# Performance work log

Measured on AMD Instinct MI355X. Metric: run time of the kernel, lower is better.

Reference implementation:

```python
import jax, jax.numpy as jnp
import numpy as np

EPS = 1e-5

def layer_norm(x, w, b):
    m = jnp.mean(x, axis=-1, keepdims=True)
    v = jnp.mean(jnp.square(x - m), axis=-1, keepdims=True)
    return (x - m) * jax.lax.rsqrt(v + EPS) * w + b

def time_shift(x):
    # shift sequence right by one, zero-pad first step: (B,L,D)
    return jnp.pad(x[:, :-1], ((0, 0), (1, 0), (0, 0)))

def wkv(time_decay, time_first, k, v):
    # Numerically-stable RWKV v4 WKV recurrence. k,v: (B,L,D)
    w = -jnp.exp(time_decay)  # (D,) negative decay
    u = time_first            # (D,)
    B, L, D = k.shape
    kT = jnp.swapaxes(k, 0, 1)  # (L,B,D)
    vT = jnp.swapaxes(v, 0, 1)
    a0 = jnp.zeros((B, D), k.dtype)
    b0 = jnp.zeros((B, D), k.dtype)
    p0 = jnp.full((B, D), -1e38, k.dtype)

    def step(carry, kv_t):
        a, b, p = carry
        k_t, v_t = kv_t
        ww = u + k_t
        q = jnp.maximum(p, ww)
        e1 = jnp.exp(p - q)
        e2 = jnp.exp(ww - q)
        out = (e1 * a + e2 * v_t) / (e1 * b + e2)
        ww2 = p + w
        q2 = jnp.maximum(ww2, k_t)
        e1b = jnp.exp(ww2 - q2)
        e2b = jnp.exp(k_t - q2)
        return (e1b * a + e2b * v_t, e1b * b + e2b, q2), out

    _, outs = jax.lax.scan(step, (a0, b0, p0), (kT, vT))
    return jnp.swapaxes(outs, 0, 1)  # (B,L,D)

def setup_inputs() -> dict:
    key = jax.random.key(0)
    B, L, D, D_att, D_ffn = 8, 2048, 1024, 1024, 4096
    ks = jax.random.split(key, 16)
    s = 1.0 / np.sqrt(D)
    inp = {
        "x": jax.random.normal(ks[0], (B, L, D), jnp.float32),
        "ln_att_w": jnp.ones((D,), jnp.float32),
        "ln_att_b": jnp.zeros((D,), jnp.float32),
        "ln_ffn_w": jnp.ones((D,), jnp.float32),
        "ln_ffn_b": jnp.zeros((D,), jnp.float32),
        "att_time_decay": jax.random.normal(ks[1], (D_att,), jnp.float32) * 0.5,
        "att_time_first": jax.random.normal(ks[2], (D_att,), jnp.float32) * 0.5,
        "att_mix_k": jax.random.uniform(ks[3], (D,), jnp.float32),
        "att_mix_v": jax.random.uniform(ks[4], (D,), jnp.float32),
        "att_mix_r": jax.random.uniform(ks[5], (D,), jnp.float32),
        "att_Wk": jax.random.normal(ks[6], (D_att, D), jnp.float32) * s,
        "att_Wv": jax.random.normal(ks[7], (D_att, D), jnp.float32) * s,
        "att_Wr": jax.random.normal(ks[8], (D_att, D), jnp.float32) * s,
        "att_Wo": jax.random.normal(ks[9], (D, D_att), jnp.float32) * s,
        "ffn_mix_k": jax.random.uniform(ks[10], (D,), jnp.float32),
        "ffn_mix_r": jax.random.uniform(ks[11], (D,), jnp.float32),
        "ffn_Wk": jax.random.normal(ks[12], (D_ffn, D), jnp.float32) * s,
        "ffn_Wv": jax.random.normal(ks[13], (D, D_ffn), jnp.float32) * (1.0 / np.sqrt(D_ffn)),
        "ffn_Wr": jax.random.normal(ks[14], (D, D), jnp.float32) * s,
    }
    return inp

def rwkv_block(x, ln_att_w, ln_att_b, ln_ffn_w, ln_ffn_b,
               att_time_decay, att_time_first, att_mix_k, att_mix_v, att_mix_r,
               att_Wk, att_Wv, att_Wr, att_Wo,
               ffn_mix_k, ffn_mix_r, ffn_Wk, ffn_Wv, ffn_Wr):
    # --- time-mix (WKV attention) ---
    xa = layer_norm(x, ln_att_w, ln_att_b)
    xs = time_shift(xa)
    k = jnp.einsum('bld,ad->bla', xa * att_mix_k + xs * (1.0 - att_mix_k), att_Wk)
    v = jnp.einsum('bld,ad->bla', xa * att_mix_v + xs * (1.0 - att_mix_v), att_Wv)
    r = jnp.einsum('bld,ad->bla', xa * att_mix_r + xs * (1.0 - att_mix_r), att_Wr)
    att = jnp.einsum('bla,da->bld', jax.nn.sigmoid(r) * wkv(att_time_decay, att_time_first, k, v), att_Wo)
    x = x + att
    # --- channel-mix FFN ---
    xf = layer_norm(x, ln_ffn_w, ln_ffn_b)
    xs = time_shift(xf)
    kx = xf * ffn_mix_k + xs * (1.0 - ffn_mix_k)
    rx = xf * ffn_mix_r + xs * (1.0 - ffn_mix_r)
    h = jnp.square(jax.nn.relu(jnp.einsum('bld,fd->blf', kx, ffn_Wk)))
    ffn = jax.nn.sigmoid(jnp.einsum('bld,ed->ble', rx, ffn_Wr)) * jnp.einsum('blf,df->bld', h, ffn_Wv)
    return x + ffn

def reference(x, ln_att_w, ln_att_b, ln_ffn_w, ln_ffn_b,
              att_time_decay, att_time_first, att_mix_k, att_mix_v, att_mix_r,
              att_Wk, att_Wv, att_Wr, att_Wo,
              ffn_mix_k, ffn_mix_r, ffn_Wk, ffn_Wv, ffn_Wr):
    return rwkv_block(x, ln_att_w, ln_att_b, ln_ffn_w, ln_ffn_b,
                      att_time_decay, att_time_first, att_mix_k, att_mix_v, att_mix_r,
                      att_Wk, att_Wv, att_Wr, att_Wo,
                      ffn_mix_k, ffn_mix_r, ffn_Wk, ffn_Wv, ffn_Wr)
```

## Files before the change

kernel.cpp:

```cpp
#include <hip/hip_runtime.h>
#include <stdint.h>

#define DDIM 1024
#define LSEQ 2048
#define BSZ  8
#define FDIM 4096
#define MROWS (BSZ*LSEQ)
#define NCHUNK 32
#define CLEN  (LSEQ/NCHUNK)

typedef float        f32x4  __attribute__((ext_vector_type(4)));
typedef unsigned int u32x4  __attribute__((ext_vector_type(4)));

using gas_void = const __attribute__((address_space(1))) void;
using las_void = __attribute__((address_space(3))) void;

__device__ __forceinline__ void gload16(const void* g, void* l) {
    __builtin_amdgcn_global_load_lds((gas_void*)g, (las_void*)l, 16, 0, 0);
}

__device__ __forceinline__ void mfma_bf16(f32x4& d, u32x4 a, u32x4 b) {
    asm("v_mfma_f32_16x16x32_bf16 %0, %1, %2, %0" : "+v"(d) : "v"(a), "v"(b));
}

__device__ __forceinline__ unsigned short f2bf(float f) {
    __bf16 h = (__bf16)f;
    return __builtin_bit_cast(unsigned short, h);
}

struct CvtArgs {
    const float* s[7];
    __bf16*      d[7];
    int          cum[8];
};

__global__ __launch_bounds__(256) void cvt_all(CvtArgs a)
{
    const int i = blockIdx.x * 256 + threadIdx.x;
    if (i >= a.cum[7]) return;
    int seg = 0;
#pragma unroll 6
    while (i >= a.cum[seg + 1]) ++seg;
    const int off = i - a.cum[seg];
    float4 f = ((const float4*)a.s[seg])[off];
    ushort4 o;
    o.x = f2bf(f.x); o.y = f2bf(f.y); o.z = f2bf(f.z); o.w = f2bf(f.w);
    ((ushort4*)a.d[seg])[off] = o;
}

__device__ __forceinline__ void blk_reduce4(float& a, float& b, float& c, float& d) {
#pragma unroll
    for (int off = 32; off >= 1; off >>= 1) {
        a += __shfl_xor(a, off, 64);
        b += __shfl_xor(b, off, 64);
        c += __shfl_xor(c, off, 64);
        d += __shfl_xor(d, off, 64);
    }
    __shared__ float sm[4][4];
    const int tid = threadIdx.x;
    if ((tid & 63) == 0) {
        sm[tid >> 6][0] = a; sm[tid >> 6][1] = b;
        sm[tid >> 6][2] = c; sm[tid >> 6][3] = d;
    }
    __syncthreads();
    a = sm[0][0] + sm[1][0] + sm[2][0] + sm[3][0];
    b = sm[0][1] + sm[1][1] + sm[2][1] + sm[3][1];
    c = sm[0][2] + sm[1][2] + sm[2][2] + sm[3][2];
    d = sm[0][3] + sm[1][3] + sm[2][3] + sm[3][3];
}

__global__ __launch_bounds__(256) void ln_mix3(
    const float* __restrict__ xin, const float* __restrict__ lnw, const float* __restrict__ lnb,
    const float* __restrict__ mkv, const float* __restrict__ mvv, const float* __restrict__ mrv,
    __bf16* __restrict__ ok, __bf16* __restrict__ ov, __bf16* __restrict__ orr)
{
    const int row = blockIdx.x;
    const int l   = row & (LSEQ - 1);
    const int tid = threadIdx.x;
    const size_t rbase = (size_t)row * DDIM;
    const float4 cur = ((const float4*)(xin + rbase))[tid];
    float4 prv = make_float4(0.f, 0.f, 0.f, 0.f);
    if (l > 0) prv = ((const float4*)(xin + rbase - DDIM))[tid];
    float s0 = cur.x + cur.y + cur.z + cur.w;
    float q0 = cur.x*cur.x + cur.y*cur.y + cur.z*cur.z + cur.w*cur.w;
    float s1 = prv.x + prv.y + prv.z + prv.w;
    float q1 = prv.x*prv.x + prv.y*prv.y + prv.z*prv.z + prv.w*prv.w;
    blk_reduce4(s0, q0, s1, q1);
    const float inv = 1.f / (float)DDIM;
    const float m0 = s0 * inv, m1 = s1 * inv;
    const float r0 = rsqrtf(fmaxf(q0 * inv - m0*m0, 0.f) + 1e-5f);
    const float r1 = rsqrtf(fmaxf(q1 * inv - m1*m1, 0.f) + 1e-5f);
    const float4 w4 = ((const float4*)lnw)[tid];
    const float4 b4 = ((const float4*)lnb)[tid];
    const float4 k4 = ((const float4*)mkv)[tid];
    const float4 v4 = ((const float4*)mvv)[tid];
    const float4 r4 = ((const float4*)mrv)[tid];
    const float cA[4] = {cur.x, cur.y, cur.z, cur.w};
    const float pA[4] = {prv.x, prv.y, prv.z, prv.w};
    const float wA[4] = {w4.x, w4.y, w4.z, w4.w};
    const float bA[4] = {b4.x, b4.y, b4.z, b4.w};
    const float kA[4] = {k4.x, k4.y, k4.z, k4.w};
    const float vA[4] = {v4.x, v4.y, v4.z, v4.w};
    const float rA[4] = {r4.x, r4.y, r4.z, r4.w};
    ushort4 pk, pv, pr;
    unsigned short* pkp = &pk.x; unsigned short* pvp = &pv.x; unsigned short* prp = &pr.x;
#pragma unroll
    for (int j = 0; j < 4; ++j) {
        float xa = (cA[j] - m0) * r0 * wA[j] + bA[j];
        float xs = (l > 0) ? ((pA[j] - m1) * r1 * wA[j] + bA[j]) : 0.f;
        pkp[j] = f2bf(xa * kA[j] + xs * (1.f - kA[j]));
        pvp[j] = f2bf(xa * vA[j] + xs * (1.f - vA[j]));
        prp[j] = f2bf(xa * rA[j] + xs * (1.f - rA[j]));
    }
    const size_t oi = (size_t)row * (DDIM/4) + tid;
    ((ushort4*)ok)[oi]  = pk;
    ((ushort4*)ov)[oi]  = pv;
    ((ushort4*)orr)[oi] = pr;
}

__global__ __launch_bounds__(256) void ln_mix2(
    const float* __restrict__ xin, const float* __restrict__ lnw, const float* __restrict__ lnb,
    const float* __restrict__ mkv, const float* __restrict__ mrv,
    __bf16* __restrict__ ok, __bf16* __restrict__ orr)
{
    const int row = blockIdx.x;
    const int l   = row & (LSEQ - 1);
    const int tid = threadIdx.x;
    const size_t rbase = (size_t)row * DDIM;
    const float4 cur = ((const float4*)(xin + rbase))[tid];
    float4 prv = make_float4(0.f, 0.f, 0.f, 0.f);
    if (l > 0) prv = ((const float4*)(xin + rbase - DDIM))[tid];
    float s0 = cur.x + cur.y + cur.z + cur.w;
    float q0 = cur.x*cur.x + cur.y*cur.y + cur.z*cur.z + cur.w*cur.w;
    float s1 = prv.x + prv.y + prv.z + prv.w;
    float q1 = prv.x*prv.x + prv.y*prv.y + prv.z*prv.z + prv.w*prv.w;
    blk_reduce4(s0, q0, s1, q1);
    const float inv = 1.f / (float)DDIM;
    const float m0 = s0 * inv, m1 = s1 * inv;
    const float r0 = rsqrtf(fmaxf(q0 * inv - m0*m0, 0.f) + 1e-5f);
    const float r1 = rsqrtf(fmaxf(q1 * inv - m1*m1, 0.f) + 1e-5f);
    const float4 w4 = ((const float4*)lnw)[tid];
    const float4 b4 = ((const float4*)lnb)[tid];
    const float4 k4 = ((const float4*)mkv)[tid];
    const float4 r4 = ((const float4*)mrv)[tid];
    const float cA[4] = {cur.x, cur.y, cur.z, cur.w};
    const float pA[4] = {prv.x, prv.y, prv.z, prv.w};
    const float wA[4] = {w4.x, w4.y, w4.z, w4.w};
    const float bA[4] = {b4.x, b4.y, b4.z, b4.w};
    const float kA[4] = {k4.x, k4.y, k4.z, k4.w};
    const float rA[4] = {r4.x, r4.y, r4.z, r4.w};
    ushort4 pk, pr;
    unsigned short* pkp = &pk.x; unsigned short* prp = &pr.x;
#pragma unroll
    for (int j = 0; j < 4; ++j) {
        float xa = (cA[j] - m0) * r0 * wA[j] + bA[j];
        float xs = (l > 0) ? ((pA[j] - m1) * r1 * wA[j] + bA[j]) : 0.f;
        pkp[j] = f2bf(xa * kA[j] + xs * (1.f - kA[j]));
        prp[j] = f2bf(xa * rA[j] + xs * (1.f - rA[j]));
    }
    const size_t oi = (size_t)row * (DDIM/4) + tid;
    ((ushort4*)ok)[oi]  = pk;
    ((ushort4*)orr)[oi] = pr;
}

__global__ __launch_bounds__(256) void wkv_phase1(
    const __bf16* __restrict__ kin, const __bf16* __restrict__ vin,
    const float* __restrict__ td,
    float* __restrict__ sa, float* __restrict__ sb, float* __restrict__ sp)
{
    const int idx = blockIdx.x * 256 + threadIdx.x;
    const int d  = idx & (DDIM - 1);
    const int bc = idx >> 10;
    const int b  = bc & (BSZ - 1);
    const int c  = bc >> 3;
    const float w = -__expf(td[d]);
    const size_t base = ((size_t)b * LSEQ + (size_t)c * CLEN) * DDIM + d;
    float a = 0.f, bbv = 0.f, p = -1e38f;
    for (int t = 0; t < CLEN; ++t) {
        const size_t off = base + (size_t)t * DDIM;
        const float kt = (float)kin[off];
        const float vt = (float)vin[off];
        const float ww2 = p + w;
        const float q2  = fmaxf(ww2, kt);
        const float e1  = __expf(ww2 - q2);
        const float e2  = __expf(kt - q2);
        a   = e1 * a   + e2 * vt;
        bbv = e1 * bbv + e2;
        p   = q2;
    }
    sa[idx] = a; sb[idx] = bbv; sp[idx] = p;
}

__global__ __launch_bounds__(256) void wkv_phase2(
    const __bf16* __restrict__ kin, const __bf16* __restrict__ vin,
    const __bf16* __restrict__ srin,
    const float* __restrict__ td, const float* __restrict__ tf,
    const float* __restrict__ sa, const float* __restrict__ sb,
    const float* __restrict__ sp,
    __bf16* __restrict__ outp)
{
    const int idx = blockIdx.x * 256 + threadIdx.x;
    const int d  = idx & (DDIM - 1);
    const int bc = idx >> 10;
    const int b  = bc & (BSZ - 1);
    const int c  = bc >> 3;
    const float w = -__expf(td[d]);
    const float u = tf[d];
    const float nw = (float)CLEN * w;

    float a = 0.f, bbv = 0.f, p = -1e38f;
    for (int j = 0; j < c; ++j) {
        const int sidx = ((j * BSZ + b) << 10) + d;
        const float aj = sa[sidx], bj = sb[sidx], pj = sp[sidx];
        const float ps = p + nw;
        const float pn = fmaxf(ps, pj);
        const float e1 = __expf(ps - pn);
        const float e2 = __expf(pj - pn);
        a   = e1 * a   + e2 * aj;
        bbv = e1 * bbv + e2 * bj;
        p   = pn;
    }

    const size_t base = ((size_t)b * LSEQ + (size_t)c * CLEN) * DDIM + d;
    for (int t = 0; t < CLEN; ++t) {
        const size_t off = base + (size_t)t * DDIM;
        const float kt = (float)kin[off];
        const float vt = (float)vin[off];
        const float sr = (float)srin[off];
        const float ww = u + kt;
        const float q  = fmaxf(p, ww);
        const float e1 = __expf(p - q);
        const float e2 = __expf(ww - q);
        const float o  = (e1 * a + e2 * vt) / (e1 * bbv + e2);
        outp[off] = (__bf16)(sr * o);
        const float ww2 = p + w;
        const float q2  = fmaxf(ww2, kt);
        const float e1b = __expf(ww2 - q2);
        const float e2b = __expf(kt - q2);
        a   = e1b * a   + e2b * vt;
        bbv = e1b * bbv + e2b;
        p   = q2;
    }
}

template<int EPI>
__global__ __launch_bounds__(512, 2)
void gemm8(const __bf16* __restrict__ A, const __bf16* __restrict__ Bw,
           float* outF, __bf16* outH,
           const float* auxF, const __bf16* __restrict__ auxH,
           int N, int K, int gy)
{
    __shared__ __align__(16) char smem[131072];
    const int tid  = threadIdx.x;
    const int lane = tid & 63;
    const int wid  = tid >> 6;
    const int wr = wid >> 2, wc = wid & 3;

    const int nwg = gridDim.x;
    const int f = blockIdx.x;
    const int g = (f & 7) * (nwg >> 3) + (f >> 3);
    const int tx = g / gy;
    const int ty = g - tx * gy;
    const size_t row0 = (size_t)tx * 256;
    const size_t col0 = (size_t)ty * 256;

    auto stage = [&](int buf, int k0, int isB, int q) {
        const int row  = q * 128 + (tid >> 2);
        const int slot = (tid & 3) ^ ((row >> 1) & 3);
        const __bf16* gp = (isB ? Bw + (col0 + row) * (size_t)K
                                : A  + (row0 + row) * (size_t)K) + k0 + slot * 8;
        char* lp = smem + buf * 32768 + isB * 16384 + q * 8192 + wid * 1024;
        gload16(gp, lp);
    };
    auto rdA = [&](int buf, int m) -> u32x4 {
        const int row  = wr * 128 + m * 16 + (lane & 15);
        const int slot = (lane >> 4) ^ ((row >> 1) & 3);
        return *(const u32x4*)(smem + buf * 32768 + row * 64 + slot * 16);
    };
    auto rdB = [&](int buf, int n) -> u32x4 {
        const int row  = wc * 64 + n * 16 + (lane & 15);
        const int slot = (lane >> 4) ^ ((row >> 1) & 3);
        return *(const u32x4*)(smem + buf * 32768 + 16384 + row * 64 + slot * 16);
    };

    f32x4 acc[8][4] = {};
    const int ns = K / 32;

    stage(0,  0, 0, 0); stage(0,  0, 0, 1); stage(0,  0, 1, 0); stage(0,  0, 1, 1);
    stage(1, 32, 0, 0); stage(1, 32, 0, 1); stage(1, 32, 1, 0); stage(1, 32, 1, 1);
    stage(2, 64, 0, 0); stage(2, 64, 0, 1); stage(2, 64, 1, 0); stage(2, 64, 1, 1);

    for (int t = 0; t < ns; ++t) {
        const int cb = t & 3;
        if (t < ns - 2)       asm volatile("s_waitcnt vmcnt(8)" ::: "memory");
        else if (t == ns - 2) asm volatile("s_waitcnt vmcnt(4)" ::: "memory");
        else                  asm volatile("s_waitcnt vmcnt(0)" ::: "memory");
        __builtin_amdgcn_s_barrier();

        const int pf = t + 3;
        const int pb = pf & 3;
        const int pk = pf * 32;

        u32x4 bfr[4];
#pragma unroll
        for (int n = 0; n < 4; ++n) bfr[n] = rdB(cb, n);
        u32x4 afr[4];
#pragma unroll
        for (int m = 0; m < 4; ++m) afr[m] = rdA(cb, m);
        if (pf < ns) { stage(pb, pk, 0, 0); stage(pb, pk, 0, 1); }
        __builtin_amdgcn_s_setprio(1);
#pragma unroll
        for (int m = 0; m < 4; ++m)
#pragma unroll
            for (int n = 0; n < 4; ++n)
                mfma_bf16(acc[m][n], afr[m], bfr[n]);
        __builtin_amdgcn_s_setprio(0);

        u32x4 afr2[4];
#pragma unroll
        for (int m = 0; m < 4; ++m) afr2[m] = rdA(cb, m + 4);
        if (pf < ns) { stage(pb, pk, 1, 0); stage(pb, pk, 1, 1); }
        __builtin_amdgcn_s_setprio(1);
#pragma unroll
        for (int m = 0; m < 4; ++m)
#pragma unroll
            for (int n = 0; n < 4; ++n)
                mfma_bf16(acc[m + 4][n], afr2[m], bfr[n]);
        __builtin_amdgcn_s_setprio(0);
    }
    asm volatile("s_nop 7\n\ts_nop 7\n\ts_nop 3");

    const size_t obr = row0 + wr * 128 + ((lane >> 4) << 2);
    const size_t obc = col0 + wc * 64 + (lane & 15);
#pragma unroll
    for (int m = 0; m < 8; ++m) {
#pragma unroll
        for (int n = 0; n < 4; ++n) {
#pragma unroll
            for (int j = 0; j < 4; ++j) {
                const size_t idx = (obr + m * 16 + j) * (size_t)N + obc + n * 16;
                const float v = acc[m][n][j];
                if constexpr (EPI == 1) {
                    outH[idx] = (__bf16)(1.f / (1.f + __expf(-v)));
                } else if constexpr (EPI == 2) {
                    const float t2 = fmaxf(v, 0.f);
                    outH[idx] = (__bf16)(t2 * t2);
                } else if constexpr (EPI == 3) {
                    outF[idx] = auxF[idx] + v;
                } else if constexpr (EPI == 4) {
                    outF[idx] = auxF[idx] + (float)auxH[idx] * v;
                } else {
                    outH[idx] = (__bf16)v;
                }
            }
        }
    }
}

extern "C" void kernel_launch(void* const* d_in, const int* in_sizes, int n_in,
                              void* d_out, int out_size, void* d_ws, size_t ws_size,
                              hipStream_t stream)
{
    const float* x    = (const float*)d_in[0];
    const float* lnaw = (const float*)d_in[1];
    const float* lnab = (const float*)d_in[2];
    const float* lnfw = (const float*)d_in[3];
    const float* lnfb = (const float*)d_in[4];
    const float* tdec = (const float*)d_in[5];
    const float* tfir = (const float*)d_in[6];
    const float* amk  = (const float*)d_in[7];
    const float* amv  = (const float*)d_in[8];
    const float* amr  = (const float*)d_in[9];
    const float* aWk  = (const float*)d_in[10];
    const float* aWv  = (const float*)d_in[11];
    const float* aWr  = (const float*)d_in[12];
    const float* aWo  = (const float*)d_in[13];
    const float* fmk  = (const float*)d_in[14];
    const float* fmr  = (const float*)d_in[15];
    const float* fWk  = (const float*)d_in[16];
    const float* fWv  = (const float*)d_in[17];
    const float* fWr  = (const float*)d_in[18];
    float* out = (float*)d_out;

    char* ws = (char*)d_ws;
    const size_t MiB = 1ull << 20;
    __bf16* Wk_h  = (__bf16*)ws;
    __bf16* Wv_h  = Wk_h + (1ull << 20);
    __bf16* Wr_h  = Wk_h + (2ull << 20);
    __bf16* Wo_h  = Wk_h + (3ull << 20);
    __bf16* fWk_h = Wk_h + (4ull << 20);
    __bf16* fWv_h = Wk_h + (8ull << 20);
    __bf16* fWr_h = Wk_h + (12ull << 20);
    __bf16* xk = (__bf16*)(ws + 26 * MiB);
    __bf16* xv = (__bf16*)(ws + 58 * MiB);
    __bf16* xr = (__bf16*)(ws + 90 * MiB);
    __bf16* kb = (__bf16*)(ws + 122 * MiB);
    __bf16* vb = (__bf16*)(ws + 154 * MiB);
    __bf16* sr = (__bf16*)(ws + 186 * MiB);
    float* st_a = (float*)(ws + 218 * MiB);
    float* st_b = (float*)(ws + 219 * MiB);
    float* st_p = (float*)(ws + 220 * MiB);
    __bf16* atta = xk;
    __bf16* kx   = xv;
    __bf16* rx   = xr;
    __bf16* sb   = xk;
    __bf16* hb   = (__bf16*)(ws + 90 * MiB);

    CvtArgs ca;
    ca.s[0] = aWk;  ca.d[0] = Wk_h;
    ca.s[1] = aWv;  ca.d[1] = Wv_h;
    ca.s[2] = aWr;  ca.d[2] = Wr_h;
    ca.s[3] = aWo;  ca.d[3] = Wo_h;
    ca.s[4] = fWk;  ca.d[4] = fWk_h;
    ca.s[5] = fWv;  ca.d[5] = fWv_h;
    ca.s[6] = fWr;  ca.d[6] = fWr_h;
    {
        const int sz[7] = {1<<18, 1<<18, 1<<18, 1<<18, 1<<20, 1<<20, 1<<18};
        int c = 0;
        for (int i = 0; i < 7; ++i) { ca.cum[i] = c; c += sz[i]; }
        ca.cum[7] = c;
    }
    cvt_all<<<(ca.cum[7] + 255) / 256, 256, 0, stream>>>(ca);

    ln_mix3<<<MROWS, 256, 0, stream>>>(x, lnaw, lnab, amk, amv, amr, xk, xv, xr);

    const int gD = (MROWS / 256) * (DDIM / 256);
    const int gF = (MROWS / 256) * (FDIM / 256);
    gemm8<5><<<gD, 512, 0, stream>>>(xk, Wk_h, nullptr, kb, nullptr, nullptr, DDIM, DDIM, DDIM/256);
    gemm8<5><<<gD, 512, 0, stream>>>(xv, Wv_h, nullptr, vb, nullptr, nullptr, DDIM, DDIM, DDIM/256);
    gemm8<1><<<gD, 512, 0, stream>>>(xr, Wr_h, nullptr, sr, nullptr, nullptr, DDIM, DDIM, DDIM/256);

    const int nthreads = BSZ * DDIM * NCHUNK;
    wkv_phase1<<<nthreads / 256, 256, 0, stream>>>(kb, vb, tdec, st_a, st_b, st_p);
    wkv_phase2<<<nthreads / 256, 256, 0, stream>>>(kb, vb, sr, tdec, tfir,
                                                   st_a, st_b, st_p, atta);

    gemm8<3><<<gD, 512, 0, stream>>>(atta, Wo_h, out, nullptr, x, nullptr, DDIM, DDIM, DDIM/256);

    ln_mix2<<<MROWS, 256, 0, stream>>>(out, lnfw, lnfb, fmk, fmr, kx, rx);

    gemm8<1><<<gD, 512, 0, stream>>>(rx, fWr_h, nullptr, sb, nullptr, nullptr, DDIM, DDIM, DDIM/256);

    gemm8<2><<<gF, 512, 0, stream>>>(kx, fWk_h, nullptr, hb, nullptr, nullptr, FDIM, DDIM, FDIM/256);

    gemm8<4><<<gD, 512, 0, stream>>>(hb, fWv_h, out, nullptr, out, sb, DDIM, FDIM, DDIM/256);
}
```

Measured before the change: 719.4 us.

## Restructure GEMM main loop into eight-phase double-buffered pipeline with K=64 tiles

Replaces the four-buffer, K=32-per-step GEMM loop with a double-buffered K=64 tile scheme split into eight phases. Each phase issues one half-tile global-to-LDS load, reads fragments, and runs 16 MFMAs between barriers. Waits are fixed vmcnt(6) points. The goal is finer interleaving of loads with MFMA work and fewer stalls from loads. Out-of-range tile loads are clamped to the last tile rather than skipped, which adds redundant traffic at the tail. The extra barriers per phase add synchronisation cost.

```diff
diff --git a/kernel.cpp b/kernel.cpp
--- a/kernel.cpp
+++ b/kernel.cpp
@@ -264,70 +264,82 @@
     const size_t row0 = (size_t)tx * 256;
     const size_t col0 = (size_t)ty * 256;
 
-    auto stage = [&](int buf, int k0, int isB, int q) {
-        const int row  = q * 128 + (tid >> 2);
-        const int slot = (tid & 3) ^ ((row >> 1) & 3);
-        const __bf16* gp = (isB ? Bw + (col0 + row) * (size_t)K
-                                : A  + (row0 + row) * (size_t)K) + k0 + slot * 8;
-        char* lp = smem + buf * 32768 + isB * 16384 + q * 8192 + wid * 1024;
-        gload16(gp, lp);
+    const int nt = K >> 6;
+    const int iters = K >> 7;
+
+    auto stage_half = [&](int d, int X, int kh, int ktile) {
+        const int kc = (ktile < nt ? ktile : nt - 1);
+        const int kg = kc * 64 + kh * 32;
+#pragma unroll
+        for (int q = 0; q < 2; ++q) {
+            const int row   = q * 128 + wid * 16 + (lane >> 2);
+            const int chunk = (lane & 3) ^ ((row >> 1) & 3);
+            const __bf16* gp = (X ? Bw + (col0 + row) * (size_t)K
+                                  : A  + (row0 + row) * (size_t)K) + kg + chunk * 8;
+            char* lp = smem + d * 65536 + X * 32768 + kh * 16384 + q * 8192 + wid * 1024;
+            gload16(gp, lp);
+        }
     };
-    auto rdA = [&](int buf, int m) -> u32x4 {
+    auto rdA = [&](int d, int ks, int m) -> u32x4 {
         const int row  = wr * 128 + m * 16 + (lane & 15);
         const int slot = (lane >> 4) ^ ((row >> 1) & 3);
-        return *(const u32x4*)(smem + buf * 32768 + row * 64 + slot * 16);
+        return *(const u32x4*)(smem + d * 65536 + ks * 16384 + row * 64 + slot * 16);
     };
-    auto rdB = [&](int buf, int n) -> u32x4 {
+    auto rdB = [&](int d, int ks, int n) -> u32x4 {
         const int row  = wc * 64 + n * 16 + (lane & 15);
         const int slot = (lane >> 4) ^ ((row >> 1) & 3);
-        return *(const u32x4*)(smem + buf * 32768 + 16384 + row * 64 + slot * 16);
+        return *(const u32x4*)(smem + d * 65536 + 32768 + ks * 16384 + row * 64 + slot * 16);
     };
 
     f32x4 acc[8][4] = {};
-    const int ns = K / 32;
-
-    stage(0,  0, 0, 0); stage(0,  0, 0, 1); stage(0,  0, 1, 0); stage(0,  0, 1, 1);
-    stage(1, 32, 0, 0); stage(1, 32, 0, 1); stage(1, 32, 1, 0); stage(1, 32, 1, 1);
-    stage(2, 64, 0, 0); stage(2, 64, 0, 1); stage(2, 64, 1, 0); stage(2, 64, 1, 1);
-
-    for (int t = 0; t < ns; ++t) {
-        const int cb = t & 3;
-        if (t < ns - 2)       asm volatile("s_waitcnt vmcnt(8)" ::: "memory");
-        else if (t == ns - 2) asm volatile("s_waitcnt vmcnt(4)" ::: "memory");
-        else                  asm volatile("s_waitcnt vmcnt(0)" ::: "memory");
-        __builtin_amdgcn_s_barrier();
-
-        const int pf = t + 3;
-        const int pb = pf & 3;
-        const int pk = pf * 32;
-
-        u32x4 bfr[4];
-#pragma unroll
-        for (int n = 0; n < 4; ++n) bfr[n] = rdB(cb, n);
-        u32x4 afr[4];
-#pragma unroll
-        for (int m = 0; m < 4; ++m) afr[m] = rdA(cb, m);
-        if (pf < ns) { stage(pb, pk, 0, 0); stage(pb, pk, 0, 1); }
-        __builtin_amdgcn_s_setprio(1);
-#pragma unroll
-        for (int m = 0; m < 4; ++m)
-#pragma unroll
-            for (int n = 0; n < 4; ++n)
-                mfma_bf16(acc[m][n], afr[m], bfr[n]);
-        __builtin_amdgcn_s_setprio(0);
-
-        u32x4 afr2[4];
-#pragma unroll
-        for (int m = 0; m < 4; ++m) afr2[m] = rdA(cb, m + 4);
-        if (pf < ns) { stage(pb, pk, 1, 0); stage(pb, pk, 1, 1); }
-        __builtin_amdgcn_s_setprio(1);
-#pragma unroll
-        for (int m = 0; m < 4; ++m)
-#pragma unroll
-            for (int n = 0; n < 4; ++n)
-                mfma_bf16(acc[m + 4][n], afr2[m], bfr[n]);
-        __builtin_amdgcn_s_setprio(0);
-    }
+    u32x4 bfr[4];
+
+#define VM6 asm volatile("s_waitcnt vmcnt(6)" ::: "memory")
+
+#define PHASE(d, ks, mh, RD8, STAGE_STMT, VMW)                                   \
+    {                                                                            \
+        u32x4 afr[4];                                                            \
+        _Pragma("unroll")                                                        \
+        for (int m = 0; m < 4; ++m) afr[m] = rdA(d, ks, (mh) * 4 + m);           \
+        if (RD8) {                                                               \
+            _Pragma("unroll")                                                    \
+            for (int n = 0; n < 4; ++n) bfr[n] = rdB(d, ks, n);                  \
+        }                                                                        \
+        STAGE_STMT;                                                              \
+        VMW;                                                                     \
+        __builtin_amdgcn_s_barrier();                                            \
+        asm volatile("s_waitcnt lgkmcnt(0)" ::: "memory");                       \
+        __builtin_amdgcn_sched_barrier(0);                                       \
+        __builtin_amdgcn_s_setprio(1);                                           \
+        _Pragma("unroll")                                                        \
+        for (int m = 0; m < 4; ++m) {                                            \
+            _Pragma("unroll")                                                    \
+            for (int n = 0; n < 4; ++n)                                          \
+                mfma_bf16(acc[(mh) * 4 + m][n], afr[m], bfr[n]);                 \
+        }                                                                        \
+        __builtin_amdgcn_s_setprio(0);                                           \
+        __builtin_amdgcn_s_barrier();                                            \
+    }
+
+    stage_half(0, 0, 0, 0); stage_half(0, 0, 1, 0);
+    stage_half(0, 1, 0, 0); stage_half(0, 1, 1, 0);
+    stage_half(1, 1, 0, 1); stage_half(1, 0, 0, 1); stage_half(1, 1, 1, 1);
+    VM6;
+    __builtin_amdgcn_s_barrier();
+
+    for (int it = 0; it < iters; ++it) {
+        const int kt = 2 * it;
+        PHASE(0, 0, 0, 1, stage_half(1, 0, 1, kt + 1), );
+        PHASE(0, 0, 1, 0, stage_half(0, 1, 0, kt + 2), );
+        PHASE(0, 1, 0, 1, stage_half(0, 0, 0, kt + 2), );
+        PHASE(0, 1, 1, 0, stage_half(0, 1, 1, kt + 2), VM6);
+        PHASE(1, 0, 0, 1, stage_half(0, 0, 1, kt + 2), );
+        PHASE(1, 0, 1, 0, stage_half(1, 1, 0, kt + 3), );
+        PHASE(1, 1, 0, 1, stage_half(1, 0, 0, kt + 3), );
+        PHASE(1, 1, 1, 0, stage_half(1, 1, 1, kt + 3), VM6);
+    }
+#undef PHASE
+#undef VM6
     asm volatile("s_nop 7\n\ts_nop 7\n\ts_nop 3");
 
     const size_t obr = row0 + wr * 128 + ((lane >> 4) << 2);
```

Measured after the change: 727.7 us. About the same (+1.2%).
